# Kernel optimization log

Hardware: AMD Instinct MI355X
Metric: run time of the kernel (lower is better)

The kernel has to match this reference:

```python
import jax, jax.numpy as jnp
import numpy as np
from math import sqrt

EMBED_DIM = 1024
NUM_HEADS = 16
HEAD_DIM = EMBED_DIM // NUM_HEADS  # 64
SCALE = sqrt(HEAD_DIM)


def _rotate_half(x):
    # matches torch: stack((-x[...,1::2], x[...,0::2]), -1).flatten(-2)
    x1 = x[..., 0::2]
    x2 = x[..., 1::2]
    return jnp.stack((-x2, x1), axis=-1).reshape(x.shape)


def _apply_rope(x, seq_len):
    # x: [B, H, S, D]
    inv_freq = 1.0 / (10000.0 ** (jnp.arange(0, HEAD_DIM, 2, dtype=jnp.float32) / HEAD_DIM))
    pos = jnp.arange(seq_len, dtype=jnp.float32)
    freqs = jnp.outer(pos, inv_freq)            # [S, D/2]
    emb = jnp.concatenate([freqs, freqs], -1)   # [S, D]
    cos = jnp.cos(emb)[None, None].astype(x.dtype)
    sin = jnp.sin(emb)[None, None].astype(x.dtype)
    return x * cos + _rotate_half(x) * sin


def setup_inputs() -> dict:
    key = jax.random.key(0)
    ks = jax.random.split(key, 9)
    B, S, E = 2, 2048, EMBED_DIM
    s = 1.0 / np.sqrt(E)
    return {
        "x": jax.random.normal(ks[0], (B, S, E), jnp.float32),
        "Wq": jax.random.uniform(ks[1], (E, E), jnp.float32, -s, s),
        "bq": jnp.zeros((E,), jnp.float32),
        "Wk": jax.random.uniform(ks[2], (E, E), jnp.float32, -s, s),
        "bk": jnp.zeros((E,), jnp.float32),
        "Wv": jax.random.uniform(ks[3], (E, E), jnp.float32, -s, s),
        "bv": jnp.zeros((E,), jnp.float32),
        "Wo": jax.random.uniform(ks[4], (E, E), jnp.float32, -s, s),
        "bo": jnp.zeros((E,), jnp.float32),
    }


def reference(x, Wq, bq, Wk, bk, Wv, bv, Wo, bo):
    B, S, E = x.shape
    H, D = NUM_HEADS, HEAD_DIM
    # projections (torch Linear: x @ W.T + b), split heads -> [B, H, S, D]
    q = (x @ Wq.T + bq).reshape(B, S, H, D).transpose(0, 2, 1, 3)
    k = (x @ Wk.T + bk).reshape(B, S, H, D).transpose(0, 2, 1, 3)
    v = (x @ Wv.T + bv).reshape(B, S, H, D).transpose(0, 2, 1, 3)
    q = _apply_rope(q, S)
    k = _apply_rope(k, S)
    attn = jnp.einsum("bhqd,bhkd->bhqk", q, k) / SCALE
    attn = jax.nn.softmax(attn, axis=-1)
    out = jnp.einsum("bhqk,bhkd->bhqd", attn, v)
    out = out.transpose(0, 2, 1, 3).reshape(B, S, E)
    return out @ Wo.T + bo
```

## Files before the change

kernel.cpp:

```cpp
#include <hip/hip_runtime.h>
#include <hip/hip_bf16.h>
#include <math.h>

typedef __bf16 bf16;
typedef __bf16 bf16x8 __attribute__((ext_vector_type(8)));
typedef float f32x4 __attribute__((ext_vector_type(4)));

#define SEQ  2048
#define EMB  1024
#define NH   16
#define HD   64
#define MTOT 4096

__device__ __forceinline__ void gl_lds16(const void* g, void* l) {
  __builtin_amdgcn_global_load_lds(
      (const __attribute__((address_space(1))) void*)g,
      (__attribute__((address_space(3))) void*)l, 16, 0, 0);
}

__device__ __forceinline__ f32x4 mfma16(bf16x8 a, bf16x8 b, f32x4 c) {
  return __builtin_amdgcn_mfma_f32_16x16x32_bf16(a, b, c, 0, 0, 0);
}

#define ROPE_C 0.41524101186092026f
#define QSCL  0.1803368801111244f

__global__ __launch_bounds__(256) void cvt_all_kernel(
    const float* __restrict__ x,
    const float* __restrict__ w0, const float* __restrict__ w1,
    const float* __restrict__ w2, const float* __restrict__ w3,
    bf16* __restrict__ dst) {
  const int y = blockIdx.y;
  const size_t WN = (size_t)EMB * EMB;
  const float* src = (y < 4) ? (x + (size_t)y * WN)
                   : (y == 4) ? w0 : (y == 5) ? w1 : (y == 6) ? w2 : w3;
  size_t i = ((size_t)blockIdx.x * 256 + threadIdx.x) * 8;
  float4 a = *(const float4*)(src + i);
  float4 b = *(const float4*)(src + i + 4);
  bf16x8 o;
  o[0] = (bf16)a.x; o[1] = (bf16)a.y; o[2] = (bf16)a.z; o[3] = (bf16)a.w;
  o[4] = (bf16)b.x; o[5] = (bf16)b.y; o[6] = (bf16)b.z; o[7] = (bf16)b.w;
  *(bf16x8*)(dst + (size_t)y * WN + i) = o;
}

__global__ __launch_bounds__(256) void gemm_kernel(
    const bf16* __restrict__ X,
    const bf16* __restrict__ W0, const bf16* __restrict__ W1, const bf16* __restrict__ W2,
    const float* __restrict__ B0, const float* __restrict__ B1, const float* __restrict__ B2,
    bf16* __restrict__ Oq, bf16* __restrict__ Ok, bf16* __restrict__ Ovt)
{
  const int K = EMB;
  const int tid  = threadIdx.x;
  const int lane = tid & 63;
  const int w    = tid >> 6;
  const int wm   = w >> 1, wn = w & 1;
  const int tile_n = blockIdx.x * 128;
  const int tile_m = blockIdx.y * 128;
  const int z = blockIdx.z;
  const bf16*  Wsel = (z == 0) ? W0 : (z == 1 ? W1 : W2);
  const float* Bsel = (z == 0) ? B0 : (z == 1 ? B1 : B2);

  __shared__ __align__(16) unsigned char smem[128 * 132 * 2];
  bf16* As = (bf16*)smem;
  bf16* Bs = (bf16*)(smem + 8192);

  f32x4 acc[4][4];
#pragma unroll
  for (int i = 0; i < 4; i++)
#pragma unroll
    for (int j = 0; j < 4; j++) acc[i][j] = f32x4{0.f, 0.f, 0.f, 0.f};

  const int quad = lane >> 4;
  const int l15  = lane & 15;
  const int srow = lane >> 2;
  const int scl  = lane & 3;

  for (int k0 = 0; k0 < K; k0 += 32) {
#pragma unroll
    for (int i = 0; i < 2; i++) {
      int r = i * 64 + w * 16 + srow;
      int c = scl ^ ((r >> 1) & 3);
      gl_lds16(X    + (size_t)(tile_m + r) * K + k0 + c * 8, As + (i * 64 + w * 16) * 32);
      gl_lds16(Wsel + (size_t)(tile_n + r) * K + k0 + c * 8, Bs + (i * 64 + w * 16) * 32);
    }
    __syncthreads();

    bf16x8 af[4], bfr[4];
#pragma unroll
    for (int mt = 0; mt < 4; mt++) {
      int ml = wm * 64 + mt * 16 + l15;
      af[mt] = *(const bf16x8*)(As + ml * 32 + (quad ^ ((ml >> 1) & 3)) * 8);
    }
#pragma unroll
    for (int nt = 0; nt < 4; nt++) {
      int nl = wn * 64 + nt * 16 + l15;
      bfr[nt] = *(const bf16x8*)(Bs + nl * 32 + (quad ^ ((nl >> 1) & 3)) * 8);
    }
#pragma unroll
    for (int mt = 0; mt < 4; mt++)
#pragma unroll
      for (int nt = 0; nt < 4; nt++)
        acc[mt][nt] = mfma16(af[mt], bfr[nt], acc[mt][nt]);
    __syncthreads();
  }

  bf16* CS = (bf16*)smem;
  const int b = tile_m >> 11;
  const int s0 = tile_m & (SEQ - 1);

  if (z < 2) {
#pragma unroll
    for (int nt = 0; nt < 4; nt++) {
      const int nl = wn * 64 + nt * 16 + l15;
      const int n = tile_n + nl;
      const float bias = Bsel[n];
      const int j = n & 31;
      const float invf = exp2f(-(float)j * ROPE_C);
#pragma unroll
      for (int mt = 0; mt < 4; mt++) {
#pragma unroll
        for (int r = 0; r < 4; r++) {
          const int ml = wm * 64 + mt * 16 + quad * 4 + r;
          float a = acc[mt][nt][r] + bias;
          float p = __shfl_xor(a, 1, 64);
          float th = (float)((s0 + ml) & (SEQ - 1)) * invf;
          float sn, cs;
          __sincosf(th, &sn, &cs);
          float res = (n & 1) ? fmaf(p, sn, a * cs) : fmaf(-p, sn, a * cs);
          if (z == 0) res *= QSCL;
          CS[ml * 132 + nl] = (bf16)res;
        }
      }
    }
    __syncthreads();
    bf16* Odst = (z == 0) ? Oq : Ok;
#pragma unroll
    for (int g = 0; g < 8; g++) {
      int unit = g * 256 + tid;
      int chunk = unit & 7;
      int row = unit >> 3;
      int hl = row >> 7, sl = row & 127;
      bf16x8 v = *(const bf16x8*)(CS + sl * 132 + hl * 64 + chunk * 8);
      int hg = (tile_n >> 6) + hl;
      size_t o = ((size_t)(b * NH + hg) * SEQ + s0 + sl) * HD + chunk * 8;
      *(bf16x8*)(Odst + o) = v;
    }
  } else {
#pragma unroll
    for (int nt = 0; nt < 4; nt++) {
      const int nl = wn * 64 + nt * 16 + l15;
      const float bias = Bsel[tile_n + nl];
#pragma unroll
      for (int mt = 0; mt < 4; mt++) {
        const int mb = wm * 64 + mt * 16 + quad * 4;
#pragma unroll
        for (int r = 0; r < 4; r++)
          CS[nl * 132 + mb + r] = (bf16)(acc[mt][nt][r] + bias);
      }
    }
    __syncthreads();
#pragma unroll
    for (int g = 0; g < 8; g++) {
      int unit = g * 256 + tid;
      int chunk = unit & 15;
      int row = unit >> 4;
      bf16x8 v = *(const bf16x8*)(CS + row * 132 + chunk * 8);
      int nglob = tile_n + row;
      int d = nglob & 63, hg = nglob >> 6;
      size_t o = ((size_t)(b * NH + hg) * HD + d) * SEQ + s0 + chunk * 8;
      *(bf16x8*)(Ovt + o) = v;
    }
  }
}

__global__ __launch_bounds__(256) void gemm_o_kernel(
    const bf16* __restrict__ X,
    const bf16* __restrict__ W,
    const float* __restrict__ Bb,
    float* __restrict__ Out)
{
  const int tid = threadIdx.x, lane = tid & 63, w = tid >> 6;
  const int tile_n = blockIdx.x * 128;
  const int tile_m = blockIdx.y * 64;
  __shared__ __align__(16) bf16 As[64 * 32];
  __shared__ __align__(16) bf16 Bs[128 * 32];

  f32x4 acc[4][2];
#pragma unroll
  for (int i = 0; i < 4; i++)
#pragma unroll
    for (int j = 0; j < 2; j++) acc[i][j] = f32x4{0.f, 0.f, 0.f, 0.f};

  const int quad = lane >> 4, l15 = lane & 15;
  const int srow = lane >> 2, scl = lane & 3;

  for (int k0 = 0; k0 < EMB; k0 += 32) {
    {
      int r = w * 16 + srow;
      int c = scl ^ ((r >> 1) & 3);
      gl_lds16(X + (size_t)(tile_m + r) * EMB + k0 + c * 8, As + (w * 16) * 32);
    }
#pragma unroll
    for (int i = 0; i < 2; i++) {
      int r = i * 64 + w * 16 + srow;
      int c = scl ^ ((r >> 1) & 3);
      gl_lds16(W + (size_t)(tile_n + r) * EMB + k0 + c * 8, Bs + (i * 64 + w * 16) * 32);
    }
    __syncthreads();

    bf16x8 af[4], bfr[2];
#pragma unroll
    for (int mt = 0; mt < 4; mt++) {
      int ml = mt * 16 + l15;
      af[mt] = *(const bf16x8*)(As + ml * 32 + (quad ^ ((ml >> 1) & 3)) * 8);
    }
#pragma unroll
    for (int nt = 0; nt < 2; nt++) {
      int nl = w * 32 + nt * 16 + l15;
      bfr[nt] = *(const bf16x8*)(Bs + nl * 32 + (quad ^ ((nl >> 1) & 3)) * 8);
    }
#pragma unroll
    for (int mt = 0; mt < 4; mt++)
#pragma unroll
      for (int nt = 0; nt < 2; nt++)
        acc[mt][nt] = mfma16(af[mt], bfr[nt], acc[mt][nt]);
    __syncthreads();
  }

#pragma unroll
  for (int nt = 0; nt < 2; nt++) {
    const int n = tile_n + w * 32 + nt * 16 + l15;
    const float bias = Bb[n];
#pragma unroll
    for (int mt = 0; mt < 4; mt++) {
#pragma unroll
      for (int r = 0; r < 4; r++) {
        const int m = tile_m + mt * 16 + quad * 4 + r;
        Out[(size_t)m * EMB + n] = acc[mt][nt][r] + bias;
      }
    }
  }
}

__global__ __launch_bounds__(256) void flash_kernel(
    const bf16* __restrict__ Q,
    const bf16* __restrict__ Kk,
    const bf16* __restrict__ Vt,
    bf16* __restrict__ O)
{
  const int bh = blockIdx.y;
  const int qt = blockIdx.x;
  const int tid = threadIdx.x, lane = tid & 63, w = tid >> 6;
  const int quad = lane >> 4, l15 = lane & 15;

  __shared__ __align__(16) unsigned char smem[65536];
  bf16* Ks = (bf16*)smem;
  bf16* Vs = (bf16*)(smem + 16384);
  bf16* Ps = (bf16*)(smem + 32768);

  const bf16* qbase = Q  + (size_t)bh * SEQ * HD;
  const bf16* kbase = Kk + (size_t)bh * SEQ * HD;
  const bf16* vbase = Vt + (size_t)bh * HD * SEQ;

  bf16x8 qf[2][2];
#pragma unroll
  for (int m = 0; m < 2; m++)
#pragma unroll
    for (int t = 0; t < 2; t++)
      qf[m][t] = *(const bf16x8*)(qbase + (size_t)(qt * 128 + w * 32 + m * 16 + l15) * HD
                                  + t * 32 + quad * 8);

  float lsum[2][4];
  f32x4 oacc[2][4];
#pragma unroll
  for (int m = 0; m < 2; m++)
#pragma unroll
    for (int i = 0; i < 4; i++) { lsum[m][i] = 0.f; oacc[m][i] = f32x4{0.f, 0.f, 0.f, 0.f}; }

  for (int kt = 0; kt < SEQ / 128; kt++) {
#pragma unroll
    for (int i = 0; i < 4; i++) {
      int r = w * 32 + i * 8 + (lane >> 3);
      int c = (lane & 7) ^ (r & 7);
      gl_lds16(kbase + (size_t)(kt * 128 + r) * HD + c * 8, Ks + (w * 32 + i * 8) * 64);
      int dv = w * 16 + i * 4 + (lane >> 4);
      int cv = (lane & 15) ^ (dv & 15);
      gl_lds16(vbase + (size_t)dv * SEQ + kt * 128 + cv * 8, Vs + (w * 16 + i * 4) * 128);
    }
    __syncthreads();

#pragma unroll
    for (int nt = 0; nt < 8; nt++) {
      int krow = nt * 16 + l15;
      bf16x8 kf[2];
#pragma unroll
      for (int t = 0; t < 2; t++)
        kf[t] = *(const bf16x8*)(Ks + krow * 64 + (((t * 4 + quad) ^ (krow & 7)) & 7) * 8);
#pragma unroll
      for (int m = 0; m < 2; m++) {
        f32x4 s = f32x4{0.f, 0.f, 0.f, 0.f};
        s = mfma16(qf[m][0], kf[0], s);
        s = mfma16(qf[m][1], kf[1], s);
#pragma unroll
        for (int r = 0; r < 4; r++) {
          float p = __builtin_amdgcn_exp2f(s[r]);
          lsum[m][r] += p;
          int row = m * 16 + quad * 4 + r;
          int col = nt * 16 + l15;
          Ps[w * 4096 + row * 128 + (((col >> 3) ^ row) & 15) * 8 + (col & 7)] = (bf16)p;
        }
      }
    }

#pragma unroll
    for (int t2 = 0; t2 < 4; t2++) {
      bf16x8 vf[4];
#pragma unroll
      for (int dt = 0; dt < 4; dt++) {
        int d = dt * 16 + l15;
        vf[dt] = *(const bf16x8*)(Vs + d * 128 + (((t2 * 4 + quad) ^ (d & 15)) & 15) * 8);
      }
#pragma unroll
      for (int m = 0; m < 2; m++) {
        int row = m * 16 + l15;
        bf16x8 pf = *(const bf16x8*)(Ps + w * 4096 + row * 128
                                     + (((t2 * 4 + quad) ^ l15) & 15) * 8);
#pragma unroll
        for (int dt = 0; dt < 4; dt++)
          oacc[m][dt] = mfma16(pf, vf[dt], oacc[m][dt]);
      }
    }
    __syncthreads();
  }

#pragma unroll
  for (int m = 0; m < 2; m++)
#pragma unroll
    for (int r = 0; r < 4; r++) {
      float s = lsum[m][r];
      s += __shfl_xor(s, 1, 64);
      s += __shfl_xor(s, 2, 64);
      s += __shfl_xor(s, 4, 64);
      s += __shfl_xor(s, 8, 64);
      lsum[m][r] = __builtin_amdgcn_rcpf(s);
    }

  const int b = bh >> 4, h = bh & 15;
#pragma unroll
  for (int m = 0; m < 2; m++)
#pragma unroll
    for (int dt = 0; dt < 4; dt++)
#pragma unroll
      for (int r = 0; r < 4; r++) {
        int srow = qt * 128 + w * 32 + m * 16 + quad * 4 + r;
        int dg = dt * 16 + l15;
        float val = oacc[m][dt][r] * lsum[m][r];
        O[((size_t)(b * SEQ + srow)) * EMB + h * HD + dg] = (bf16)val;
      }
}

extern "C" void kernel_launch(void* const* d_in, const int* in_sizes, int n_in,
                              void* d_out, int out_size, void* d_ws, size_t ws_size,
                              hipStream_t stream) {
  const float* x  = (const float*)d_in[0];
  const float* Wq = (const float*)d_in[1];
  const float* bq = (const float*)d_in[2];
  const float* Wk = (const float*)d_in[3];
  const float* bk = (const float*)d_in[4];
  const float* Wv = (const float*)d_in[5];
  const float* bv = (const float*)d_in[6];
  const float* Wo = (const float*)d_in[7];
  const float* bo = (const float*)d_in[8];

  const size_t XN = (size_t)MTOT * EMB;
  const size_t WN = (size_t)EMB * EMB;

  bf16* xb = (bf16*)d_ws;
  bf16* wq = xb + XN;
  bf16* wk = wq + WN;
  bf16* wv = wk + WN;
  bf16* wo = wv + WN;
  bf16* q  = wo + WN;
  bf16* k  = q + XN;
  bf16* vt = k + XN;
  bf16* at = vt + XN;
  float* out = (float*)d_out;

  dim3 blk(256);
  cvt_all_kernel<<<dim3(512, 8), blk, 0, stream>>>(x, Wq, Wk, Wv, Wo, xb);

  gemm_kernel<<<dim3(8, 32, 3), blk, 0, stream>>>(
      xb, wq, wk, wv, bq, bk, bv, q, k, vt);
  flash_kernel<<<dim3(16, 32), blk, 0, stream>>>(q, k, vt, at);
  gemm_o_kernel<<<dim3(8, 64), blk, 0, stream>>>(at, wo, bo, out);
}
```

Before: 214.4 us.

## Double-buffer K/V tiles and keep P in registers via transposed S=K·Q^T

The flash attention kernel now double-buffers the K and V tiles in LDS, issuing the async global-to-LDS loads for the next key tile before computing on the current one. This removes one barrier per iteration and overlaps memory latency with compute. It also computes S as K·Q^T so the exponentiated probabilities already sit in the MFMA operand layout, which lets P feed the PV MFMA straight from registers and drops the P round-trip through LDS. V fragments are gathered as two 4-wide reads to match that layout, and output stores are vectorised to 4 bf16. The cost is twice the LDS for K/V, more register pressure, and a reliance on an MFMA operand-layout permutation being correct.

```diff
diff --git a/kernel.cpp b/kernel.cpp
--- a/kernel.cpp
+++ b/kernel.cpp
@@ -3,6 +3,7 @@
 #include <math.h>
 
 typedef __bf16 bf16;
+typedef __bf16 bf16x4 __attribute__((ext_vector_type(4)));
 typedef __bf16 bf16x8 __attribute__((ext_vector_type(8)));
 typedef float f32x4 __attribute__((ext_vector_type(4)));
 
@@ -254,30 +255,14 @@
   const int quad = lane >> 4, l15 = lane & 15;
 
   __shared__ __align__(16) unsigned char smem[65536];
-  bf16* Ks = (bf16*)smem;
-  bf16* Vs = (bf16*)(smem + 16384);
-  bf16* Ps = (bf16*)(smem + 32768);
 
   const bf16* qbase = Q  + (size_t)bh * SEQ * HD;
   const bf16* kbase = Kk + (size_t)bh * SEQ * HD;
   const bf16* vbase = Vt + (size_t)bh * HD * SEQ;
 
-  bf16x8 qf[2][2];
-#pragma unroll
-  for (int m = 0; m < 2; m++)
-#pragma unroll
-    for (int t = 0; t < 2; t++)
-      qf[m][t] = *(const bf16x8*)(qbase + (size_t)(qt * 128 + w * 32 + m * 16 + l15) * HD
-                                  + t * 32 + quad * 8);
-
-  float lsum[2][4];
-  f32x4 oacc[2][4];
-#pragma unroll
-  for (int m = 0; m < 2; m++)
-#pragma unroll
-    for (int i = 0; i < 4; i++) { lsum[m][i] = 0.f; oacc[m][i] = f32x4{0.f, 0.f, 0.f, 0.f}; }
-
-  for (int kt = 0; kt < SEQ / 128; kt++) {
+  auto stage = [&](int kt, int buf) {
+    bf16* Ks = (bf16*)(smem + buf * 32768);
+    bf16* Vs = Ks + 8192;
 #pragma unroll
     for (int i = 0; i < 4; i++) {
       int r = w * 32 + i * 8 + (lane >> 3);
@@ -287,76 +272,93 @@
       int cv = (lane & 15) ^ (dv & 15);
       gl_lds16(vbase + (size_t)dv * SEQ + kt * 128 + cv * 8, Vs + (w * 16 + i * 4) * 128);
     }
-    __syncthreads();
-
-#pragma unroll
-    for (int nt = 0; nt < 8; nt++) {
-      int krow = nt * 16 + l15;
-      bf16x8 kf[2];
-#pragma unroll
-      for (int t = 0; t < 2; t++)
-        kf[t] = *(const bf16x8*)(Ks + krow * 64 + (((t * 4 + quad) ^ (krow & 7)) & 7) * 8);
-#pragma unroll
-      for (int m = 0; m < 2; m++) {
-        f32x4 s = f32x4{0.f, 0.f, 0.f, 0.f};
-        s = mfma16(qf[m][0], kf[0], s);
-        s = mfma16(qf[m][1], kf[1], s);
-#pragma unroll
-        for (int r = 0; r < 4; r++) {
-          float p = __builtin_amdgcn_exp2f(s[r]);
-          lsum[m][r] += p;
-          int row = m * 16 + quad * 4 + r;
-          int col = nt * 16 + l15;
-          Ps[w * 4096 + row * 128 + (((col >> 3) ^ row) & 15) * 8 + (col & 7)] = (bf16)p;
+  };
+
+  stage(0, 0);
+
+  bf16x8 qf[2][2];
+#pragma unroll
+  for (int m = 0; m < 2; m++)
+#pragma unroll
+    for (int t = 0; t < 2; t++)
+      qf[m][t] = *(const bf16x8*)(qbase + (size_t)(qt * 128 + w * 32 + m * 16 + l15) * HD
+                                  + t * 32 + quad * 8);
+
+  float lsum[2] = {0.f, 0.f};
+  f32x4 oacc[2][4];
+#pragma unroll
+  for (int m = 0; m < 2; m++)
+#pragma unroll
+    for (int i = 0; i < 4; i++) oacc[m][i] = f32x4{0.f, 0.f, 0.f, 0.f};
+
+  __syncthreads();
+
+  for (int kt = 0; kt < SEQ / 128; kt++) {
+    const int buf = kt & 1;
+    if (kt + 1 < SEQ / 128) stage(kt + 1, buf ^ 1);
+    const bf16* Ks = (const bf16*)(smem + buf * 32768);
+    const bf16* Vs = Ks + 8192;
+
+#pragma unroll
+    for (int t2 = 0; t2 < 4; t2++) {
+      bf16x8 pa[2];
+#pragma unroll
+      for (int hh = 0; hh < 2; hh++) {
+        const int krow = (t2 * 2 + hh) * 16 + l15;
+        const int swz = krow & 7;
+        bf16x8 kf0 = *(const bf16x8*)(Ks + krow * 64 + ((quad ^ swz) & 7) * 8);
+        bf16x8 kf1 = *(const bf16x8*)(Ks + krow * 64 + (((4 + quad) ^ swz) & 7) * 8);
+#pragma unroll
+        for (int mq = 0; mq < 2; mq++) {
+          f32x4 s = f32x4{0.f, 0.f, 0.f, 0.f};
+          s = mfma16(kf0, qf[mq][0], s);
+          s = mfma16(kf1, qf[mq][1], s);
+#pragma unroll
+          for (int r = 0; r < 4; r++) {
+            float p = __builtin_amdgcn_exp2f(s[r]);
+            lsum[mq] += p;
+            pa[mq][hh * 4 + r] = (bf16)p;
+          }
         }
       }
-    }
-
-#pragma unroll
-    for (int t2 = 0; t2 < 4; t2++) {
-      bf16x8 vf[4];
 #pragma unroll
       for (int dt = 0; dt < 4; dt++) {
-        int d = dt * 16 + l15;
-        vf[dt] = *(const bf16x8*)(Vs + d * 128 + (((t2 * 4 + quad) ^ (d & 15)) & 15) * 8);
-      }
-#pragma unroll
-      for (int m = 0; m < 2; m++) {
-        int row = m * 16 + l15;
-        bf16x8 pf = *(const bf16x8*)(Ps + w * 4096 + row * 128
-                                     + (((t2 * 4 + quad) ^ l15) & 15) * 8);
-#pragma unroll
-        for (int dt = 0; dt < 4; dt++)
-          oacc[m][dt] = mfma16(pf, vf[dt], oacc[m][dt]);
-      }
-    }
-    __syncthreads();
-  }
-
-#pragma unroll
-  for (int m = 0; m < 2; m++)
-#pragma unroll
-    for (int r = 0; r < 4; r++) {
-      float s = lsum[m][r];
-      s += __shfl_xor(s, 1, 64);
-      s += __shfl_xor(s, 2, 64);
-      s += __shfl_xor(s, 4, 64);
-      s += __shfl_xor(s, 8, 64);
-      lsum[m][r] = __builtin_amdgcn_rcpf(s);
-    }
+        const int d = dt * 16 + l15;
+        const bf16* vrow = Vs + d * 128 + (quad & 1) * 4;
+        const int G = t2 * 4 + (quad >> 1);
+        bf16x4 va = *(const bf16x4*)(vrow + ((G ^ l15) & 15) * 8);
+        bf16x4 vb = *(const bf16x4*)(vrow + (((G + 2) ^ l15) & 15) * 8);
+        bf16x8 vv = __builtin_shufflevector(va, vb, 0, 1, 2, 3, 4, 5, 6, 7);
+#pragma unroll
+        for (int mq = 0; mq < 2; mq++)
+          oacc[mq][dt] = mfma16(vv, pa[mq], oacc[mq][dt]);
+      }
+    }
+    __syncthreads();
+  }
+
+  float rls[2];
+#pragma unroll
+  for (int mq = 0; mq < 2; mq++) {
+    float s = lsum[mq];
+    s += __shfl_xor(s, 16, 64);
+    s += __shfl_xor(s, 32, 64);
+    rls[mq] = __builtin_amdgcn_rcpf(s);
+  }
 
   const int b = bh >> 4, h = bh & 15;
 #pragma unroll
-  for (int m = 0; m < 2; m++)
-#pragma unroll
-    for (int dt = 0; dt < 4; dt++)
-#pragma unroll
-      for (int r = 0; r < 4; r++) {
-        int srow = qt * 128 + w * 32 + m * 16 + quad * 4 + r;
-        int dg = dt * 16 + l15;
-        float val = oacc[m][dt][r] * lsum[m][r];
-        O[((size_t)(b * SEQ + srow)) * EMB + h * HD + dg] = (bf16)val;
-      }
+  for (int mq = 0; mq < 2; mq++) {
+    const int srow = qt * 128 + w * 32 + mq * 16 + l15;
+    bf16* orow = O + ((size_t)(b * SEQ + srow)) * EMB + h * HD;
+#pragma unroll
+    for (int dt = 0; dt < 4; dt++) {
+      bf16x4 ov;
+#pragma unroll
+      for (int r = 0; r < 4; r++) ov[r] = (bf16)(oacc[mq][dt][r] * rls[mq]);
+      *(bf16x4*)(orow + dt * 16 + quad * 4) = ov;
+    }
+  }
 }
 
 extern "C" void kernel_launch(void* const* d_in, const int* in_sizes, int n_in,
```

Measured after the change: 205.0 us. 4.4% less time.
